# Kernel tuning notes

Measured on AMD Instinct MI355X. Metric: run time of the kernel, lower is better.

## Reference

```python
import jax, jax.numpy as jnp
import numpy as np

SCALE = 64.0
MARGIN = 0.5
EPS_CLAMP = 1e-7
EPS_NORM = 1e-12

N, D, C = 4096, 512, 30000


def setup_inputs() -> dict:
    key = jax.random.key(0)
    k1, k2, k3 = jax.random.split(key, 3)
    embeddings = jax.random.normal(k1, (N, D), dtype=jnp.float32)
    classifier_weights = jax.random.normal(k2, (C, D), dtype=jnp.float32)
    labels = jax.random.randint(k3, (N,), 0, C, dtype=jnp.int64)
    return {"embeddings": embeddings, "labels": labels, "classifier_weights": classifier_weights}


def reference(embeddings, labels, classifier_weights):
    # F.normalize(classifier_weights): L2-normalize each class row (dim=1)
    norm = jnp.linalg.norm(classifier_weights, axis=1, keepdims=True)
    w_norm = classifier_weights / jnp.maximum(norm, EPS_NORM)
    # cosine similarity logits: [N, C]  (embeddings are NOT normalized in source)
    cosine = jnp.einsum("nd,cd->nc", embeddings, w_norm)
    # angle with margin added only at the target class
    angle = jnp.arccos(jnp.clip(cosine, -1.0 + EPS_CLAMP, 1.0 - EPS_CLAMP))
    one_hot = jax.nn.one_hot(labels, C, dtype=cosine.dtype)
    logits = jnp.cos(angle + MARGIN * one_hot) * SCALE
    # mean cross-entropy
    logp = jax.nn.log_softmax(logits, axis=-1)
    nll = -jnp.take_along_axis(logp, labels[:, None], axis=1)[:, 0]
    return jnp.mean(nll)
```

## Files before the change

kernel.cpp:

```cpp
#include <hip/hip_runtime.h>
#include <cstdint>
#include <cstddef>

#define N_ROWS 4096
#define DIM    512
#define NCLS   30000
#define BM 256
#define BN 256
#define BK 32
#define NT2  118
#define CPAD (NT2 * 256)
#define SPT 2
#define NSTRIPS (NT2 / SPT)
#define KT  (DIM / BK)
#define NS  (SPT * KT)

typedef float  f32x4  __attribute__((ext_vector_type(4)));
typedef short  bf16x8 __attribute__((ext_vector_type(8)));
typedef unsigned int   u32;
typedef unsigned short u16;

#define WB_BYTES   ((size_t)CPAD * DIM * 2)
#define EB_BYTES   ((size_t)N_ROWS * DIM * 2)
#define PS_BYTES   ((size_t)NT2 * N_ROWS * 4)
#define CT_BYTES   ((size_t)N_ROWS * 4)
#define BL_BYTES   (64 * 4)
#define LAB_BYTES  ((size_t)N_ROWS * 4)

#define CLIP_HI ( 1.0f - 1e-7f)
#define CLIP_LO (-1.0f + 1e-7f)
#define COSM 0.8775825618903728f
#define SINM 0.4794255386042030f
#define K1   92.33248261972189f

__device__ __forceinline__ u16 f2bf(float f) {
  u32 x = __builtin_bit_cast(u32, f);
  x += 0x7fffu + ((x >> 16) & 1u);
  return (u16)(x >> 16);
}

__device__ __forceinline__ void gl_lds16(const u16* g, u16* l) {
  __builtin_amdgcn_global_load_lds((const __attribute__((address_space(1))) u32*)g,
                                   (__attribute__((address_space(3))) u32*)l,
                                   16, 0, 0);
}

__global__ void lab_detect(const int* __restrict__ lab, int* __restrict__ flag) {
  __shared__ int s_nz;
  int tid = threadIdx.x;
  if (tid == 0) s_nz = 0;
  __syncthreads();
  int nz = 0;
  for (int i = tid; i < N_ROWS / 2; i += 1024) nz |= lab[2 * i + 1];
  if (nz) atomicOr(&s_nz, 1);
  __syncthreads();
  if (tid == 0) *flag = (s_nz == 0) ? 1 : 0;
}

__global__ void lab_fix(const int* __restrict__ lab, const int* __restrict__ flag,
                        int* __restrict__ out) {
  int i = blockIdx.x * 256 + threadIdx.x;
  out[i] = flag[0] ? lab[2 * i] : lab[i];
}

__global__ void prep_w(const float* __restrict__ w, u16* __restrict__ wb) {
  int wv   = threadIdx.x >> 6;
  int lane = threadIdx.x & 63;
  int c = blockIdx.x * 4 + wv;
  u16* dst = wb + (size_t)c * DIM + lane * 8;
  if (c >= NCLS) {
    *(uint4*)dst = make_uint4(0, 0, 0, 0);
    return;
  }
  const float* src = w + (size_t)c * DIM + lane * 8;
  float4 v0 = *(const float4*)src;
  float4 v1 = *(const float4*)(src + 4);
  float a[8] = {v0.x, v0.y, v0.z, v0.w, v1.x, v1.y, v1.z, v1.w};
  float ss = 0.f;
  #pragma unroll
  for (int i = 0; i < 8; i++) ss += a[i] * a[i];
  #pragma unroll
  for (int off = 32; off; off >>= 1) ss += __shfl_xor(ss, off, 64);
  float inv = 1.0f / fmaxf(sqrtf(ss), 1e-12f);
  union { u16 h[8]; uint4 q; } pk;
  #pragma unroll
  for (int i = 0; i < 8; i++) pk.h[i] = f2bf(a[i] * inv);
  *(uint4*)dst = pk.q;
}

__global__ void prep_e(const float* __restrict__ e, u16* __restrict__ eb) {
  size_t idx = ((size_t)blockIdx.x * 256 + threadIdx.x) * 8;
  float4 v0 = *(const float4*)(e + idx);
  float4 v1 = *(const float4*)(e + idx + 4);
  float a[8] = {v0.x, v0.y, v0.z, v0.w, v1.x, v1.y, v1.z, v1.w};
  union { u16 h[8]; uint4 q; } pk;
  #pragma unroll
  for (int i = 0; i < 8; i++) pk.h[i] = f2bf(a[i]);
  *(uint4*)(eb + idx) = pk.q;
}

__global__ void tgt_k(const float* __restrict__ emb, const float* __restrict__ wts,
                      const int* __restrict__ lab, float* __restrict__ ct) {
  int w = threadIdx.x >> 6, l = threadIdx.x & 63;
  int row = blockIdx.x * 4 + w;
  int c = lab[row];
  const float* e  = emb + (size_t)row * DIM + l * 8;
  const float* wp = wts + (size_t)c   * DIM + l * 8;
  float4 e0 = *(const float4*)e,       e1 = *(const float4*)(e + 4);
  float4 w0 = *(const float4*)wp,      w1 = *(const float4*)(wp + 4);
  float dot = e0.x*w0.x + e0.y*w0.y + e0.z*w0.z + e0.w*w0.w
            + e1.x*w1.x + e1.y*w1.y + e1.z*w1.z + e1.w*w1.w;
  float ss  = w0.x*w0.x + w0.y*w0.y + w0.z*w0.z + w0.w*w0.w
            + w1.x*w1.x + w1.y*w1.y + w1.z*w1.z + w1.w*w1.w;
  #pragma unroll
  for (int off = 32; off; off >>= 1) {
    dot += __shfl_xor(dot, off, 64);
    ss  += __shfl_xor(ss,  off, 64);
  }
  if (l == 0) ct[row] = dot / fmaxf(sqrtf(ss), 1e-12f);
}

__global__ __launch_bounds__(512, 2) void arc_main(
    const u16* __restrict__ eb, const u16* __restrict__ wb,
    float* __restrict__ psum)
{
  __shared__ __align__(16) u16 lA[3][BM * BK];
  __shared__ __align__(16) u16 lB[3][BN * BK];
  __shared__ float ep[4][BM];
  const int tid = threadIdx.x;
  const int l   = tid & 63;
  const int w   = tid >> 6;
  const int wm  = w >> 2, wn = w & 3;
  const int mi    = blockIdx.x & 15;
  const int strip = blockIdx.x >> 4;
  const int rowbase = mi * BM;
  const int n0 = strip * SPT;

  u32 aoff[8], boff[4];
  const int bq = l >> 4;
  #pragma unroll
  for (int m = 0; m < 8; m++) {
    int r = wm * 128 + m * 16 + (l & 15);
    aoff[m] = (u32)r * BK + ((bq ^ ((r >> 1) & 3)) << 3);
  }
  #pragma unroll
  for (int n = 0; n < 4; n++) {
    int r = wn * 64 + n * 16 + (l & 15);
    boff[n] = (u32)r * BK + ((bq ^ ((r >> 1) & 3)) << 3);
  }

  const int sch = (w & 3) * 4;
  u32 goff[4];
  #pragma unroll
  for (int i = 0; i < 4; i++) {
    int rl = (sch + i) * 16 + (l >> 2);
    goff[i] = (u32)rl * DIM + (((l & 3) ^ ((rl >> 1) & 3)) << 3);
  }
  const bool isA = (w < 4);
  const u16* gsrc = isA ? (eb + (size_t)rowbase * DIM) : wb;
  u16* lds0 = isA ? &lA[0][0] : &lB[0][0];

  #define STAGE(u_) do {                                                     \
    const int buf_ = (u_) % 3;                                               \
    const u32 base_ = isA ? (u32)(((u_) & 15) * BK)                          \
        : (u32)(n0 + ((u_) >> 4)) * BN * DIM + (u32)(((u_) & 15) * BK);      \
    u16* dst_ = lds0 + buf_ * (BM * BK) + sch * 512;                         \
    _Pragma("unroll")                                                        \
    for (int i_ = 0; i_ < 4; i_++)                                           \
      gl_lds16(gsrc + base_ + goff[i_], dst_ + i_ * 512);                    \
  } while (0)

  f32x4 acc[8][4];
  #pragma unroll
  for (int m = 0; m < 8; m++)
    #pragma unroll
    for (int n = 0; n < 4; n++)
      #pragma unroll
      for (int q = 0; q < 4; q++) acc[m][n][q] = 0.f;

  STAGE(0);
  STAGE(1);

  for (int u = 0; u < NS; u++) {
    if (u < NS - 1) asm volatile("s_waitcnt vmcnt(4)" ::: "memory");
    else            asm volatile("s_waitcnt vmcnt(0)" ::: "memory");
    __builtin_amdgcn_s_barrier();
    asm volatile("" ::: "memory");
    if (u + 2 < NS) STAGE(u + 2);

    const int buf = u % 3;
    bf16x8 af[8], bg[4];
    #pragma unroll
    for (int m = 0; m < 8; m++) af[m] = *(const bf16x8*)&lA[buf][aoff[m]];
    #pragma unroll
    for (int n = 0; n < 4; n++) bg[n] = *(const bf16x8*)&lB[buf][boff[n]];

    __builtin_amdgcn_s_setprio(1);
    #pragma unroll
    for (int m = 0; m < 8; m++)
      #pragma unroll
      for (int n = 0; n < 4; n++)
        acc[m][n] = __builtin_amdgcn_mfma_f32_16x16x32_bf16(af[m], bg[n], acc[m][n], 0, 0, 0);
    __builtin_amdgcn_s_setprio(0);

    if ((u & 15) == 15) {
      const int nt = n0 + (u >> 4);
      #pragma unroll
      for (int m = 0; m < 8; m++) {
        #pragma unroll
        for (int q = 0; q < 4; q++) {
          float s = 0.f;
          #pragma unroll
          for (int n = 0; n < 4; n++) {
            float tc = __builtin_amdgcn_fmed3f(acc[m][n][q], CLIP_LO, CLIP_HI);
            s += __builtin_amdgcn_exp2f(__builtin_fmaf(tc, K1, -K1));
            acc[m][n][q] = 0.f;
          }
          s += __shfl_xor(s, 1, 64);
          s += __shfl_xor(s, 2, 64);
          s += __shfl_xor(s, 4, 64);
          s += __shfl_xor(s, 8, 64);
          if ((l & 15) == 0) ep[wn][wm * 128 + m * 16 + (l >> 4) * 4 + q] = s;
        }
      }
      asm volatile("s_waitcnt lgkmcnt(0)" ::: "memory");
      __builtin_amdgcn_s_barrier();
      asm volatile("" ::: "memory");
      if (l < 32) {
        int r = w * 32 + l;
        float t = ep[0][r] + ep[1][r] + ep[2][r] + ep[3][r];
        psum[(size_t)nt * N_ROWS + rowbase + r] = t;
      }
    }
  }
  #undef STAGE
}

__global__ void arc_finish1(const float* __restrict__ psum, const float* __restrict__ ct,
                            float* __restrict__ bl) {
  int tid = threadIdx.x;
  int row = blockIdx.x * 256 + tid;
  float S = 0.f;
  for (int p = 0; p < NT2; p++) S += psum[(size_t)p * N_ROWS + row];
  float c  = __builtin_amdgcn_fmed3f(ct[row], CLIP_LO, CLIP_HI);
  float cm = c * COSM - sqrtf(fmaxf(1.0f - c * c, 0.0f)) * SINM;
  float S2 = S - __builtin_amdgcn_exp2f(__builtin_fmaf(c,  K1, -K1))
               + __builtin_amdgcn_exp2f(__builtin_fmaf(cm, K1, -K1));
  float loss = 64.0f + __builtin_amdgcn_logf(S2) * 0.6931471805599453f - 64.0f * cm;
  #pragma unroll
  for (int off = 32; off; off >>= 1) loss += __shfl_xor(loss, off, 64);
  __shared__ float red[4];
  if ((tid & 63) == 0) red[tid >> 6] = loss;
  __syncthreads();
  if (tid == 0) bl[blockIdx.x] = red[0] + red[1] + red[2] + red[3];
}

__global__ void arc_finish2(const float* __restrict__ bl, float* __restrict__ out) {
  if (threadIdx.x == 0) {
    float t = 0.f;
    for (int i = 0; i < N_ROWS / 256; i++) t += bl[i];
    out[0] = t * (1.0f / (float)N_ROWS);
  }
}

extern "C" void kernel_launch(void* const* d_in, const int* in_sizes, int n_in,
                              void* d_out, int out_size, void* d_ws, size_t ws_size,
                              hipStream_t stream) {
  const float* emb   = (const float*)d_in[0];
  const int*   lab   = (const int*)d_in[1];
  const float* wts   = (const float*)d_in[2];

  char* ws = (char*)d_ws;
  u16*   wb    = (u16*)(ws);
  u16*   eb    = (u16*)(ws + WB_BYTES);
  float* psum  = (float*)(ws + WB_BYTES + EB_BYTES);
  float* ct    = (float*)(ws + WB_BYTES + EB_BYTES + PS_BYTES);
  float* bl    = (float*)(ws + WB_BYTES + EB_BYTES + PS_BYTES + CT_BYTES);
  int*   lab32 = (int*)  (ws + WB_BYTES + EB_BYTES + PS_BYTES + CT_BYTES + BL_BYTES);
  int*   flag  = (int*)  (ws + WB_BYTES + EB_BYTES + PS_BYTES + CT_BYTES + BL_BYTES + LAB_BYTES);

  lab_detect<<<dim3(1), dim3(1024), 0, stream>>>(lab, flag);
  lab_fix<<<dim3(N_ROWS / 256), dim3(256), 0, stream>>>(lab, flag, lab32);
  prep_w<<<dim3(CPAD / 4), dim3(256), 0, stream>>>(wts, wb);
  prep_e<<<dim3((N_ROWS * DIM / 8) / 256), dim3(256), 0, stream>>>(emb, eb);
  tgt_k<<<dim3(N_ROWS / 4), dim3(256), 0, stream>>>(emb, wts, lab32, ct);
  arc_main<<<dim3(16 * NSTRIPS), dim3(512), 0, stream>>>(eb, wb, psum);
  arc_finish1<<<dim3(N_ROWS / 256), dim3(256), 0, stream>>>(psum, ct, bl);
  arc_finish2<<<dim3(1), dim3(64), 0, stream>>>(bl, (float*)d_out);
}
```

Before: 214.8 us.

## Split GEMM k-step into four phases interleaving LDS reads, global stages, and MFMA

Restructures the main GEMM loop so each k-step runs in four MFMA phases. Each phase is preceded by a subset of LDS fragment reads and one quarter of the next-next stage's global-to-LDS copies, and is separated by barriers and sched_barriers with raised priority. All eight waves now share every A and B copy instead of splitting by wave role, and the triple buffers rotate via pointer swaps. The goal is to overlap memory traffic with matrix work and lower register pressure by holding only half the A fragments at once. The cost is many more workgroup barriers per k-step.

```diff
diff --git a/kernel.cpp b/kernel.cpp
--- a/kernel.cpp
+++ b/kernel.cpp
@@ -124,8 +124,7 @@
     const u16* __restrict__ eb, const u16* __restrict__ wb,
     float* __restrict__ psum)
 {
-  __shared__ __align__(16) u16 lA[3][BM * BK];
-  __shared__ __align__(16) u16 lB[3][BN * BK];
+  __shared__ __align__(16) u16 lds[6 * 8192];
   __shared__ float ep[4][BM];
   const int tid = threadIdx.x;
   const int l   = tid & 63;
@@ -134,7 +133,7 @@
   const int mi    = blockIdx.x & 15;
   const int strip = blockIdx.x >> 4;
   const int rowbase = mi * BM;
-  const int n0 = strip * SPT;
+  const int n0s = strip * SPT;
 
   u32 aoff[8], boff[4];
   const int bq = l >> 4;
@@ -149,26 +148,22 @@
     boff[n] = (u32)r * BK + ((bq ^ ((r >> 1) & 3)) << 3);
   }
 
-  const int sch = (w & 3) * 4;
-  u32 goff[4];
-  #pragma unroll
-  for (int i = 0; i < 4; i++) {
-    int rl = (sch + i) * 16 + (l >> 2);
-    goff[i] = (u32)rl * DIM + (((l & 3) ^ ((rl >> 1) & 3)) << 3);
-  }
-  const bool isA = (w < 4);
-  const u16* gsrc = isA ? (eb + (size_t)rowbase * DIM) : wb;
-  u16* lds0 = isA ? &lA[0][0] : &lB[0][0];
-
-  #define STAGE(u_) do {                                                     \
-    const int buf_ = (u_) % 3;                                               \
-    const u32 base_ = isA ? (u32)(((u_) & 15) * BK)                          \
-        : (u32)(n0 + ((u_) >> 4)) * BN * DIM + (u32)(((u_) & 15) * BK);      \
-    u16* dst_ = lds0 + buf_ * (BM * BK) + sch * 512;                         \
-    _Pragma("unroll")                                                        \
-    for (int i_ = 0; i_ < 4; i_++)                                           \
-      gl_lds16(gsrc + base_ + goff[i_], dst_ + i_ * 512);                    \
-  } while (0)
+  u32 goff[2];
+  #pragma unroll
+  for (int c = 0; c < 2; c++) {
+    int rl = c * 128 + (tid >> 2);
+    goff[c] = (u32)rl * DIM + (((tid & 3) ^ ((rl >> 1) & 3)) << 3);
+  }
+  const u16* ebR = eb + (size_t)rowbase * DIM;
+
+  u16 *pA = lds,             *qA = lds + 8192,  *sA = lds + 16384;
+  u16 *pB = lds + 24576,     *qB = lds + 32768, *sB = lds + 40960;
+
+  #define STAGE_A(v_, t_, c_) \
+    gl_lds16(ebR + (u32)(((v_) & 15) * BK) + goff[c_], (t_) + (c_) * 4096 + w * 512)
+  #define STAGE_B(v_, t_, c_) \
+    gl_lds16(wb + (u32)(n0s + ((v_) >> 4)) * (BN * DIM) + (u32)(((v_) & 15) * BK) + goff[c_], \
+             (t_) + (c_) * 4096 + w * 512)
 
   f32x4 acc[8][4];
   #pragma unroll
@@ -178,33 +173,80 @@
       #pragma unroll
       for (int q = 0; q < 4; q++) acc[m][n][q] = 0.f;
 
-  STAGE(0);
-  STAGE(1);
+  STAGE_A(0, pA, 0); STAGE_A(0, pA, 1); STAGE_B(0, pB, 0); STAGE_B(0, pB, 1);
+  STAGE_A(1, qA, 0); STAGE_A(1, qA, 1); STAGE_B(1, qB, 0); STAGE_B(1, qB, 1);
 
   for (int u = 0; u < NS; u++) {
+    const bool st = (u + 2 < NS);
+    bf16x8 afv[4], bgv[4];
+
     if (u < NS - 1) asm volatile("s_waitcnt vmcnt(4)" ::: "memory");
     else            asm volatile("s_waitcnt vmcnt(0)" ::: "memory");
-    __builtin_amdgcn_s_barrier();
-    asm volatile("" ::: "memory");
-    if (u + 2 < NS) STAGE(u + 2);
-
-    const int buf = u % 3;
-    bf16x8 af[8], bg[4];
-    #pragma unroll
-    for (int m = 0; m < 8; m++) af[m] = *(const bf16x8*)&lA[buf][aoff[m]];
-    #pragma unroll
-    for (int n = 0; n < 4; n++) bg[n] = *(const bf16x8*)&lB[buf][boff[n]];
-
+    #pragma unroll
+    for (int m = 0; m < 4; m++) afv[m] = *(const bf16x8*)&pA[aoff[m]];
+    bgv[0] = *(const bf16x8*)&pB[boff[0]];
+    bgv[1] = *(const bf16x8*)&pB[boff[1]];
+    if (st) STAGE_A(u + 2, sA, 0);
+    __builtin_amdgcn_s_barrier();
+    asm volatile("s_waitcnt lgkmcnt(0)" ::: "memory");
+    __builtin_amdgcn_sched_barrier(0);
     __builtin_amdgcn_s_setprio(1);
     #pragma unroll
-    for (int m = 0; m < 8; m++)
-      #pragma unroll
-      for (int n = 0; n < 4; n++)
-        acc[m][n] = __builtin_amdgcn_mfma_f32_16x16x32_bf16(af[m], bg[n], acc[m][n], 0, 0, 0);
+    for (int m = 0; m < 4; m++)
+      #pragma unroll
+      for (int n = 0; n < 2; n++)
+        acc[m][n] = __builtin_amdgcn_mfma_f32_16x16x32_bf16(afv[m], bgv[n], acc[m][n], 0, 0, 0);
     __builtin_amdgcn_s_setprio(0);
+    __builtin_amdgcn_sched_barrier(0);
+    __builtin_amdgcn_s_barrier();
+
+    bgv[2] = *(const bf16x8*)&pB[boff[2]];
+    bgv[3] = *(const bf16x8*)&pB[boff[3]];
+    if (st) STAGE_A(u + 2, sA, 1);
+    __builtin_amdgcn_s_barrier();
+    asm volatile("s_waitcnt lgkmcnt(0)" ::: "memory");
+    __builtin_amdgcn_sched_barrier(0);
+    __builtin_amdgcn_s_setprio(1);
+    #pragma unroll
+    for (int m = 0; m < 4; m++)
+      #pragma unroll
+      for (int n = 2; n < 4; n++)
+        acc[m][n] = __builtin_amdgcn_mfma_f32_16x16x32_bf16(afv[m], bgv[n], acc[m][n], 0, 0, 0);
+    __builtin_amdgcn_s_setprio(0);
+    __builtin_amdgcn_sched_barrier(0);
+    __builtin_amdgcn_s_barrier();
+
+    #pragma unroll
+    for (int m = 0; m < 4; m++) afv[m] = *(const bf16x8*)&pA[aoff[m + 4]];
+    if (st) STAGE_B(u + 2, sB, 0);
+    __builtin_amdgcn_s_barrier();
+    asm volatile("s_waitcnt lgkmcnt(0)" ::: "memory");
+    __builtin_amdgcn_sched_barrier(0);
+    __builtin_amdgcn_s_setprio(1);
+    #pragma unroll
+    for (int m = 0; m < 4; m++)
+      #pragma unroll
+      for (int n = 0; n < 2; n++)
+        acc[m + 4][n] = __builtin_amdgcn_mfma_f32_16x16x32_bf16(afv[m], bgv[n], acc[m + 4][n], 0, 0, 0);
+    __builtin_amdgcn_s_setprio(0);
+    __builtin_amdgcn_sched_barrier(0);
+    __builtin_amdgcn_s_barrier();
+
+    if (st) STAGE_B(u + 2, sB, 1);
+    __builtin_amdgcn_s_barrier();
+    __builtin_amdgcn_sched_barrier(0);
+    __builtin_amdgcn_s_setprio(1);
+    #pragma unroll
+    for (int m = 0; m < 4; m++)
+      #pragma unroll
+      for (int n = 2; n < 4; n++)
+        acc[m + 4][n] = __builtin_amdgcn_mfma_f32_16x16x32_bf16(afv[m], bgv[n], acc[m + 4][n], 0, 0, 0);
+    __builtin_amdgcn_s_setprio(0);
+    __builtin_amdgcn_sched_barrier(0);
+    __builtin_amdgcn_s_barrier();
 
     if ((u & 15) == 15) {
-      const int nt = n0 + (u >> 4);
+      const int nt = n0s + (u >> 4);
       #pragma unroll
       for (int m = 0; m < 8; m++) {
         #pragma unroll
@@ -231,9 +273,14 @@
         float t = ep[0][r] + ep[1][r] + ep[2][r] + ep[3][r];
         psum[(size_t)nt * N_ROWS + rowbase + r] = t;
       }
+      __builtin_amdgcn_s_barrier();
     }
-  }
-  #undef STAGE
+
+    u16* t0 = pA; pA = qA; qA = sA; sA = t0;
+    u16* t1 = pB; pB = qB; qB = sB; sB = t1;
+  }
+  #undef STAGE_A
+  #undef STAGE_B
 }
 
 __global__ void arc_finish1(const float* __restrict__ psum, const float* __restrict__ ct,
```

Result: slower. 225.3 us (+4.9%).

## Restructure GEMM mainloop to BK=64 double-buffer with interleaved load/MFMA phases

Applied to the files above, without the earlier changes.

Doubles the K tile to 64 and replaces the 3-stage ring buffer with a 2-stage double buffer. Each K step is split into four barrier-separated phases, each interleaving a slice of the next tile's global-to-LDS loads with 16 MFMAs. Occupancy is reduced to one block per CU to fit the larger LDS footprint, and the LDS swizzle switches to an XOR over 8 chunks. The aim is to cut barrier and waitcnt overhead per FLOP and overlap memory traffic with compute, at the cost of more barriers per step, lower occupancy and only one tile of prefetch depth.

```diff
diff --git a/kernel.cpp b/kernel.cpp
--- a/kernel.cpp
+++ b/kernel.cpp
@@ -7,7 +7,7 @@
 #define NCLS   30000
 #define BM 256
 #define BN 256
-#define BK 32
+#define BK 64
 #define NT2  118
 #define CPAD (NT2 * 256)
 #define SPT 2
@@ -120,55 +120,44 @@
   if (l == 0) ct[row] = dot / fmaxf(sqrtf(ss), 1e-12f);
 }
 
-__global__ __launch_bounds__(512, 2) void arc_main(
+__global__ __launch_bounds__(512, 1) void arc_main(
     const u16* __restrict__ eb, const u16* __restrict__ wb,
     float* __restrict__ psum)
 {
-  __shared__ __align__(16) u16 lA[3][BM * BK];
-  __shared__ __align__(16) u16 lB[3][BN * BK];
+  __shared__ __align__(16) u16 lds[2][2][BM * BK];
   __shared__ float ep[4][BM];
-  const int tid = threadIdx.x;
-  const int l   = tid & 63;
-  const int w   = tid >> 6;
+  const int t   = threadIdx.x;
+  const int l   = t & 63;
+  const int w   = t >> 6;
   const int wm  = w >> 2, wn = w & 3;
+  const int cl  = l & 15, bq = l >> 4;
   const int mi    = blockIdx.x & 15;
   const int strip = blockIdx.x >> 4;
   const int rowbase = mi * BM;
-  const int n0 = strip * SPT;
-
-  u32 aoff[8], boff[4];
-  const int bq = l >> 4;
-  #pragma unroll
-  for (int m = 0; m < 8; m++) {
-    int r = wm * 128 + m * 16 + (l & 15);
-    aoff[m] = (u32)r * BK + ((bq ^ ((r >> 1) & 3)) << 3);
-  }
-  #pragma unroll
-  for (int n = 0; n < 4; n++) {
-    int r = wn * 64 + n * 16 + (l & 15);
-    boff[n] = (u32)r * BK + ((bq ^ ((r >> 1) & 3)) << 3);
-  }
-
-  const int sch = (w & 3) * 4;
+  const int n0s = strip * SPT;
+
+  u32 aoff[16], boff[8];
+  #pragma unroll
+  for (int s = 0; s < 2; s++) {
+    #pragma unroll
+    for (int m = 0; m < 8; m++) {
+      int r = wm * 128 + m * 16 + cl;
+      aoff[s * 8 + m] = (u32)r * BK + (((s * 4 + bq) ^ (r & 7)) << 3);
+    }
+    #pragma unroll
+    for (int n = 0; n < 4; n++) {
+      int r = wn * 64 + n * 16 + cl;
+      boff[s * 4 + n] = (u32)r * BK + (((s * 4 + bq) ^ (r & 7)) << 3);
+    }
+  }
+
   u32 goff[4];
   #pragma unroll
-  for (int i = 0; i < 4; i++) {
-    int rl = (sch + i) * 16 + (l >> 2);
-    goff[i] = (u32)rl * DIM + (((l & 3) ^ ((rl >> 1) & 3)) << 3);
-  }
-  const bool isA = (w < 4);
-  const u16* gsrc = isA ? (eb + (size_t)rowbase * DIM) : wb;
-  u16* lds0 = isA ? &lA[0][0] : &lB[0][0];
-
-  #define STAGE(u_) do {                                                     \
-    const int buf_ = (u_) % 3;                                               \
-    const u32 base_ = isA ? (u32)(((u_) & 15) * BK)                          \
-        : (u32)(n0 + ((u_) >> 4)) * BN * DIM + (u32)(((u_) & 15) * BK);      \
-    u16* dst_ = lds0 + buf_ * (BM * BK) + sch * 512;                         \
-    _Pragma("unroll")                                                        \
-    for (int i_ = 0; i_ < 4; i_++)                                           \
-      gl_lds16(gsrc + base_ + goff[i_], dst_ + i_ * 512);                    \
-  } while (0)
+  for (int c = 0; c < 4; c++) {
+    int rl = c * 64 + (t >> 3);
+    goff[c] = (u32)rl * DIM + (((t & 7) ^ (rl & 7)) << 3);
+  }
+  const u16* ebR = eb + (size_t)rowbase * DIM;
 
   f32x4 acc[8][4];
   #pragma unroll
@@ -178,33 +167,149 @@
       #pragma unroll
       for (int q = 0; q < 4; q++) acc[m][n][q] = 0.f;
 
-  STAGE(0);
-  STAGE(1);
+  {
+    const u32 bb0 = (u32)n0s * (BN * DIM);
+    #pragma unroll
+    for (int c = 0; c < 4; c++) {
+      gl_lds16(ebR + goff[c],       &lds[0][0][c * 4096 + w * 512]);
+      gl_lds16(wb + bb0 + goff[c],  &lds[0][1][c * 4096 + w * 512]);
+    }
+  }
 
   for (int u = 0; u < NS; u++) {
-    if (u < NS - 1) asm volatile("s_waitcnt vmcnt(4)" ::: "memory");
-    else            asm volatile("s_waitcnt vmcnt(0)" ::: "memory");
+    const int bi = u & 1;
+    const u16* As = &lds[bi][0][0];
+    const u16* Bs = &lds[bi][1][0];
+    u16* An = &lds[bi ^ 1][0][0];
+    u16* Bn = &lds[bi ^ 1][1][0];
+    const bool st = (u + 1 < NS);
+    const u32 k0n = (u32)(((u + 1) & 7) * BK);
+    const u32 bbn = (u32)(n0s + ((u + 1) >> 3)) * (BN * DIM);
+
+    asm volatile("s_waitcnt vmcnt(0)" ::: "memory");
     __builtin_amdgcn_s_barrier();
     asm volatile("" ::: "memory");
-    if (u + 2 < NS) STAGE(u + 2);
-
-    const int buf = u % 3;
-    bf16x8 af[8], bg[4];
-    #pragma unroll
-    for (int m = 0; m < 8; m++) af[m] = *(const bf16x8*)&lA[buf][aoff[m]];
-    #pragma unroll
-    for (int n = 0; n < 4; n++) bg[n] = *(const bf16x8*)&lB[buf][boff[n]];
-
+
+    bf16x8 a0, a1, a2, a3, b0, b1, b2, b3;
+
+    a0 = *(const bf16x8*)&As[aoff[0]];  a1 = *(const bf16x8*)&As[aoff[1]];
+    a2 = *(const bf16x8*)&As[aoff[2]];  a3 = *(const bf16x8*)&As[aoff[3]];
+    b0 = *(const bf16x8*)&Bs[boff[0]];  b1 = *(const bf16x8*)&Bs[boff[1]];
+    b2 = *(const bf16x8*)&Bs[boff[2]];  b3 = *(const bf16x8*)&Bs[boff[3]];
+    if (st) {
+      gl_lds16(ebR + k0n + goff[0],      An + w * 512);
+      gl_lds16(wb + bbn + k0n + goff[0], Bn + w * 512);
+    }
+    __builtin_amdgcn_s_barrier();
+    asm volatile("s_waitcnt lgkmcnt(0)" ::: "memory");
     __builtin_amdgcn_s_setprio(1);
-    #pragma unroll
-    for (int m = 0; m < 8; m++)
-      #pragma unroll
-      for (int n = 0; n < 4; n++)
-        acc[m][n] = __builtin_amdgcn_mfma_f32_16x16x32_bf16(af[m], bg[n], acc[m][n], 0, 0, 0);
+    acc[0][0] = __builtin_amdgcn_mfma_f32_16x16x32_bf16(a0, b0, acc[0][0], 0, 0, 0);
+    acc[0][1] = __builtin_amdgcn_mfma_f32_16x16x32_bf16(a0, b1, acc[0][1], 0, 0, 0);
+    acc[0][2] = __builtin_amdgcn_mfma_f32_16x16x32_bf16(a0, b2, acc[0][2], 0, 0, 0);
+    acc[0][3] = __builtin_amdgcn_mfma_f32_16x16x32_bf16(a0, b3, acc[0][3], 0, 0, 0);
+    acc[1][0] = __builtin_amdgcn_mfma_f32_16x16x32_bf16(a1, b0, acc[1][0], 0, 0, 0);
+    acc[1][1] = __builtin_amdgcn_mfma_f32_16x16x32_bf16(a1, b1, acc[1][1], 0, 0, 0);
+    acc[1][2] = __builtin_amdgcn_mfma_f32_16x16x32_bf16(a1, b2, acc[1][2], 0, 0, 0);
+    acc[1][3] = __builtin_amdgcn_mfma_f32_16x16x32_bf16(a1, b3, acc[1][3], 0, 0, 0);
+    acc[2][0] = __builtin_amdgcn_mfma_f32_16x16x32_bf16(a2, b0, acc[2][0], 0, 0, 0);
+    acc[2][1] = __builtin_amdgcn_mfma_f32_16x16x32_bf16(a2, b1, acc[2][1], 0, 0, 0);
+    acc[2][2] = __builtin_amdgcn_mfma_f32_16x16x32_bf16(a2, b2, acc[2][2], 0, 0, 0);
+    acc[2][3] = __builtin_amdgcn_mfma_f32_16x16x32_bf16(a2, b3, acc[2][3], 0, 0, 0);
+    acc[3][0] = __builtin_amdgcn_mfma_f32_16x16x32_bf16(a3, b0, acc[3][0], 0, 0, 0);
+    acc[3][1] = __builtin_amdgcn_mfma_f32_16x16x32_bf16(a3, b1, acc[3][1], 0, 0, 0);
+    acc[3][2] = __builtin_amdgcn_mfma_f32_16x16x32_bf16(a3, b2, acc[3][2], 0, 0, 0);
+    acc[3][3] = __builtin_amdgcn_mfma_f32_16x16x32_bf16(a3, b3, acc[3][3], 0, 0, 0);
     __builtin_amdgcn_s_setprio(0);
-
-    if ((u & 15) == 15) {
-      const int nt = n0 + (u >> 4);
+    __builtin_amdgcn_s_barrier();
+
+    a0 = *(const bf16x8*)&As[aoff[4]];  a1 = *(const bf16x8*)&As[aoff[5]];
+    a2 = *(const bf16x8*)&As[aoff[6]];  a3 = *(const bf16x8*)&As[aoff[7]];
+    if (st) {
+      gl_lds16(ebR + k0n + goff[1],      An + 4096 + w * 512);
+      gl_lds16(wb + bbn + k0n + goff[1], Bn + 4096 + w * 512);
+    }
+    __builtin_amdgcn_s_barrier();
+    asm volatile("s_waitcnt lgkmcnt(0)" ::: "memory");
+    __builtin_amdgcn_s_setprio(1);
+    acc[4][0] = __builtin_amdgcn_mfma_f32_16x16x32_bf16(a0, b0, acc[4][0], 0, 0, 0);
+    acc[4][1] = __builtin_amdgcn_mfma_f32_16x16x32_bf16(a0, b1, acc[4][1], 0, 0, 0);
+    acc[4][2] = __builtin_amdgcn_mfma_f32_16x16x32_bf16(a0, b2, acc[4][2], 0, 0, 0);
+    acc[4][3] = __builtin_amdgcn_mfma_f32_16x16x32_bf16(a0, b3, acc[4][3], 0, 0, 0);
+    acc[5][0] = __builtin_amdgcn_mfma_f32_16x16x32_bf16(a1, b0, acc[5][0], 0, 0, 0);
+    acc[5][1] = __builtin_amdgcn_mfma_f32_16x16x32_bf16(a1, b1, acc[5][1], 0, 0, 0);
+    acc[5][2] = __builtin_amdgcn_mfma_f32_16x16x32_bf16(a1, b2, acc[5][2], 0, 0, 0);
+    acc[5][3] = __builtin_amdgcn_mfma_f32_16x16x32_bf16(a1, b3, acc[5][3], 0, 0, 0);
+    acc[6][0] = __builtin_amdgcn_mfma_f32_16x16x32_bf16(a2, b0, acc[6][0], 0, 0, 0);
+    acc[6][1] = __builtin_amdgcn_mfma_f32_16x16x32_bf16(a2, b1, acc[6][1], 0, 0, 0);
+    acc[6][2] = __builtin_amdgcn_mfma_f32_16x16x32_bf16(a2, b2, acc[6][2], 0, 0, 0);
+    acc[6][3] = __builtin_amdgcn_mfma_f32_16x16x32_bf16(a2, b3, acc[6][3], 0, 0, 0);
+    acc[7][0] = __builtin_amdgcn_mfma_f32_16x16x32_bf16(a3, b0, acc[7][0], 0, 0, 0);
+    acc[7][1] = __builtin_amdgcn_mfma_f32_16x16x32_bf16(a3, b1, acc[7][1], 0, 0, 0);
+    acc[7][2] = __builtin_amdgcn_mfma_f32_16x16x32_bf16(a3, b2, acc[7][2], 0, 0, 0);
+    acc[7][3] = __builtin_amdgcn_mfma_f32_16x16x32_bf16(a3, b3, acc[7][3], 0, 0, 0);
+    __builtin_amdgcn_s_setprio(0);
+    __builtin_amdgcn_s_barrier();
+
+    a0 = *(const bf16x8*)&As[aoff[8]];  a1 = *(const bf16x8*)&As[aoff[9]];
+    a2 = *(const bf16x8*)&As[aoff[10]]; a3 = *(const bf16x8*)&As[aoff[11]];
+    b0 = *(const bf16x8*)&Bs[boff[4]];  b1 = *(const bf16x8*)&Bs[boff[5]];
+    b2 = *(const bf16x8*)&Bs[boff[6]];  b3 = *(const bf16x8*)&Bs[boff[7]];
+    if (st) {
+      gl_lds16(ebR + k0n + goff[2],      An + 8192 + w * 512);
+      gl_lds16(wb + bbn + k0n + goff[2], Bn + 8192 + w * 512);
+    }
+    __builtin_amdgcn_s_barrier();
+    asm volatile("s_waitcnt lgkmcnt(0)" ::: "memory");
+    __builtin_amdgcn_s_setprio(1);
+    acc[0][0] = __builtin_amdgcn_mfma_f32_16x16x32_bf16(a0, b0, acc[0][0], 0, 0, 0);
+    acc[0][1] = __builtin_amdgcn_mfma_f32_16x16x32_bf16(a0, b1, acc[0][1], 0, 0, 0);
+    acc[0][2] = __builtin_amdgcn_mfma_f32_16x16x32_bf16(a0, b2, acc[0][2], 0, 0, 0);
+    acc[0][3] = __builtin_amdgcn_mfma_f32_16x16x32_bf16(a0, b3, acc[0][3], 0, 0, 0);
+    acc[1][0] = __builtin_amdgcn_mfma_f32_16x16x32_bf16(a1, b0, acc[1][0], 0, 0, 0);
+    acc[1][1] = __builtin_amdgcn_mfma_f32_16x16x32_bf16(a1, b1, acc[1][1], 0, 0, 0);
+    acc[1][2] = __builtin_amdgcn_mfma_f32_16x16x32_bf16(a1, b2, acc[1][2], 0, 0, 0);
+    acc[1][3] = __builtin_amdgcn_mfma_f32_16x16x32_bf16(a1, b3, acc[1][3], 0, 0, 0);
+    acc[2][0] = __builtin_amdgcn_mfma_f32_16x16x32_bf16(a2, b0, acc[2][0], 0, 0, 0);
+    acc[2][1] = __builtin_amdgcn_mfma_f32_16x16x32_bf16(a2, b1, acc[2][1], 0, 0, 0);
+    acc[2][2] = __builtin_amdgcn_mfma_f32_16x16x32_bf16(a2, b2, acc[2][2], 0, 0, 0);
+    acc[2][3] = __builtin_amdgcn_mfma_f32_16x16x32_bf16(a2, b3, acc[2][3], 0, 0, 0);
+    acc[3][0] = __builtin_amdgcn_mfma_f32_16x16x32_bf16(a3, b0, acc[3][0], 0, 0, 0);
+    acc[3][1] = __builtin_amdgcn_mfma_f32_16x16x32_bf16(a3, b1, acc[3][1], 0, 0, 0);
+    acc[3][2] = __builtin_amdgcn_mfma_f32_16x16x32_bf16(a3, b2, acc[3][2], 0, 0, 0);
+    acc[3][3] = __builtin_amdgcn_mfma_f32_16x16x32_bf16(a3, b3, acc[3][3], 0, 0, 0);
+    __builtin_amdgcn_s_setprio(0);
+    __builtin_amdgcn_s_barrier();
+
+    a0 = *(const bf16x8*)&As[aoff[12]]; a1 = *(const bf16x8*)&As[aoff[13]];
+    a2 = *(const bf16x8*)&As[aoff[14]]; a3 = *(const bf16x8*)&As[aoff[15]];
+    if (st) {
+      gl_lds16(ebR + k0n + goff[3],      An + 12288 + w * 512);
+      gl_lds16(wb + bbn + k0n + goff[3], Bn + 12288 + w * 512);
+    }
+    __builtin_amdgcn_s_barrier();
+    asm volatile("s_waitcnt lgkmcnt(0)" ::: "memory");
+    __builtin_amdgcn_s_setprio(1);
+    acc[4][0] = __builtin_amdgcn_mfma_f32_16x16x32_bf16(a0, b0, acc[4][0], 0, 0, 0);
+    acc[4][1] = __builtin_amdgcn_mfma_f32_16x16x32_bf16(a0, b1, acc[4][1], 0, 0, 0);
+    acc[4][2] = __builtin_amdgcn_mfma_f32_16x16x32_bf16(a0, b2, acc[4][2], 0, 0, 0);
+    acc[4][3] = __builtin_amdgcn_mfma_f32_16x16x32_bf16(a0, b3, acc[4][3], 0, 0, 0);
+    acc[5][0] = __builtin_amdgcn_mfma_f32_16x16x32_bf16(a1, b0, acc[5][0], 0, 0, 0);
+    acc[5][1] = __builtin_amdgcn_mfma_f32_16x16x32_bf16(a1, b1, acc[5][1], 0, 0, 0);
+    acc[5][2] = __builtin_amdgcn_mfma_f32_16x16x32_bf16(a1, b2, acc[5][2], 0, 0, 0);
+    acc[5][3] = __builtin_amdgcn_mfma_f32_16x16x32_bf16(a1, b3, acc[5][3], 0, 0, 0);
+    acc[6][0] = __builtin_amdgcn_mfma_f32_16x16x32_bf16(a2, b0, acc[6][0], 0, 0, 0);
+    acc[6][1] = __builtin_amdgcn_mfma_f32_16x16x32_bf16(a2, b1, acc[6][1], 0, 0, 0);
+    acc[6][2] = __builtin_amdgcn_mfma_f32_16x16x32_bf16(a2, b2, acc[6][2], 0, 0, 0);
+    acc[6][3] = __builtin_amdgcn_mfma_f32_16x16x32_bf16(a2, b3, acc[6][3], 0, 0, 0);
+    acc[7][0] = __builtin_amdgcn_mfma_f32_16x16x32_bf16(a3, b0, acc[7][0], 0, 0, 0);
+    acc[7][1] = __builtin_amdgcn_mfma_f32_16x16x32_bf16(a3, b1, acc[7][1], 0, 0, 0);
+    acc[7][2] = __builtin_amdgcn_mfma_f32_16x16x32_bf16(a3, b2, acc[7][2], 0, 0, 0);
+    acc[7][3] = __builtin_amdgcn_mfma_f32_16x16x32_bf16(a3, b3, acc[7][3], 0, 0, 0);
+    __builtin_amdgcn_s_setprio(0);
+    __builtin_amdgcn_s_barrier();
+
+    if ((u & 7) == 7) {
+      const int nt = n0s + (u >> 3);
       #pragma unroll
       for (int m = 0; m < 8; m++) {
         #pragma unroll
@@ -228,12 +333,12 @@
       asm volatile("" ::: "memory");
       if (l < 32) {
         int r = w * 32 + l;
-        float t = ep[0][r] + ep[1][r] + ep[2][r] + ep[3][r];
-        psum[(size_t)nt * N_ROWS + rowbase + r] = t;
+        float v = ep[0][r] + ep[1][r] + ep[2][r] + ep[3][r];
+        psum[(size_t)nt * N_ROWS + rowbase + r] = v;
       }
-    }
-  }
-  #undef STAGE
+      __builtin_amdgcn_s_barrier();
+    }
+  }
 }
 
 __global__ void arc_finish1(const float* __restrict__ psum, const float* __restrict__ ct,
```

Measured after the change: 213.4 us. No clear change (-0.7%).

## Shrink main GEMM tile to 128x256 with 4 waves and double buffering

Applied to the files above, without the earlier changes.

Restructures the fused cosine-logit GEMM from 256x256 tiles with 8 waves, triple buffering and two class strips per block, to 128x256 tiles with 4 waves, double buffering and one strip per block. Each block now does a single K loop and one exp/row-sum epilogue. The grid grows from 944 to 3776 blocks, which should give better load balance and occupancy. The cost is more global traffic per FLOP because the smaller M tile gives less reuse, and a shallower prefetch pipeline that waits on vmcnt(0) every iteration.

```diff
diff --git a/kernel.cpp b/kernel.cpp
--- a/kernel.cpp
+++ b/kernel.cpp
@@ -5,15 +5,13 @@
 #define N_ROWS 4096
 #define DIM    512
 #define NCLS   30000
-#define BM 256
+#define BM 128
 #define BN 256
 #define BK 32
 #define NT2  118
 #define CPAD (NT2 * 256)
-#define SPT 2
-#define NSTRIPS (NT2 / SPT)
-#define KT  (DIM / BK)
-#define NS  (SPT * KT)
+#define MI   (N_ROWS / BM)
+#define KS   (DIM / BK)
 
 typedef float  f32x4  __attribute__((ext_vector_type(4)));
 typedef short  bf16x8 __attribute__((ext_vector_type(8)));
@@ -120,55 +118,45 @@
   if (l == 0) ct[row] = dot / fmaxf(sqrtf(ss), 1e-12f);
 }
 
-__global__ __launch_bounds__(512, 2) void arc_main(
+__global__ __launch_bounds__(256) void arc_main(
     const u16* __restrict__ eb, const u16* __restrict__ wb,
     float* __restrict__ psum)
 {
-  __shared__ __align__(16) u16 lA[3][BM * BK];
-  __shared__ __align__(16) u16 lB[3][BN * BK];
+  __shared__ __align__(16) u16 lds[2][(BM + BN) * BK];
   __shared__ float ep[4][BM];
-  const int tid = threadIdx.x;
-  const int l   = tid & 63;
-  const int w   = tid >> 6;
-  const int wm  = w >> 2, wn = w & 3;
-  const int mi    = blockIdx.x & 15;
-  const int strip = blockIdx.x >> 4;
+  const int t  = threadIdx.x;
+  const int l  = t & 63;
+  const int w  = t >> 6;
+  const int cl = l & 15, bq = l >> 4;
+  const int mi    = blockIdx.x & (MI - 1);
+  const int strip = blockIdx.x >> 5;
   const int rowbase = mi * BM;
-  const int n0 = strip * SPT;
 
   u32 aoff[8], boff[4];
-  const int bq = l >> 4;
   #pragma unroll
   for (int m = 0; m < 8; m++) {
-    int r = wm * 128 + m * 16 + (l & 15);
+    int r = m * 16 + cl;
     aoff[m] = (u32)r * BK + ((bq ^ ((r >> 1) & 3)) << 3);
   }
   #pragma unroll
   for (int n = 0; n < 4; n++) {
-    int r = wn * 64 + n * 16 + (l & 15);
-    boff[n] = (u32)r * BK + ((bq ^ ((r >> 1) & 3)) << 3);
-  }
-
-  const int sch = (w & 3) * 4;
-  u32 goff[4];
-  #pragma unroll
-  for (int i = 0; i < 4; i++) {
-    int rl = (sch + i) * 16 + (l >> 2);
-    goff[i] = (u32)rl * DIM + (((l & 3) ^ ((rl >> 1) & 3)) << 3);
-  }
-  const bool isA = (w < 4);
-  const u16* gsrc = isA ? (eb + (size_t)rowbase * DIM) : wb;
-  u16* lds0 = isA ? &lA[0][0] : &lB[0][0];
-
-  #define STAGE(u_) do {                                                     \
-    const int buf_ = (u_) % 3;                                               \
-    const u32 base_ = isA ? (u32)(((u_) & 15) * BK)                          \
-        : (u32)(n0 + ((u_) >> 4)) * BN * DIM + (u32)(((u_) & 15) * BK);      \
-    u16* dst_ = lds0 + buf_ * (BM * BK) + sch * 512;                         \
-    _Pragma("unroll")                                                        \
-    for (int i_ = 0; i_ < 4; i_++)                                           \
-      gl_lds16(gsrc + base_ + goff[i_], dst_ + i_ * 512);                    \
-  } while (0)
+    int r = w * 64 + n * 16 + cl;
+    boff[n] = (u32)(BM * BK) + (u32)r * BK + ((bq ^ ((r >> 1) & 3)) << 3);
+  }
+
+  u32 ga[2], gb[4];
+  #pragma unroll
+  for (int i = 0; i < 2; i++) {
+    int rl = (w * 2 + i) * 16 + (l >> 2);
+    ga[i] = (u32)rl * DIM + (((l & 3) ^ ((rl >> 1) & 3)) << 3);
+  }
+  #pragma unroll
+  for (int j = 0; j < 4; j++) {
+    int rl = (w * 4 + j) * 16 + (l >> 2);
+    gb[j] = (u32)rl * DIM + (((l & 3) ^ ((rl >> 1) & 3)) << 3);
+  }
+  const u16* ebR = eb + (size_t)rowbase * DIM;
+  const u16* wbN = wb + (size_t)strip * BN * DIM;
 
   f32x4 acc[8][4];
   #pragma unroll
@@ -178,22 +166,32 @@
       #pragma unroll
       for (int q = 0; q < 4; q++) acc[m][n][q] = 0.f;
 
-  STAGE(0);
-  STAGE(1);
-
-  for (int u = 0; u < NS; u++) {
-    if (u < NS - 1) asm volatile("s_waitcnt vmcnt(4)" ::: "memory");
-    else            asm volatile("s_waitcnt vmcnt(0)" ::: "memory");
+  #pragma unroll
+  for (int i = 0; i < 2; i++) gl_lds16(ebR + ga[i], &lds[0][(w * 2 + i) * 512]);
+  #pragma unroll
+  for (int j = 0; j < 4; j++) gl_lds16(wbN + gb[j], &lds[0][BM * BK + (w * 4 + j) * 512]);
+
+  for (int u = 0; u < KS; u++) {
+    asm volatile("s_waitcnt vmcnt(0)" ::: "memory");
     __builtin_amdgcn_s_barrier();
     asm volatile("" ::: "memory");
-    if (u + 2 < NS) STAGE(u + 2);
-
-    const int buf = u % 3;
+
+    if (u + 1 < KS) {
+      const u32 ko = (u32)(u + 1) * BK;
+      u16* Ad = &lds[(u + 1) & 1][0];
+      u16* Bd = &lds[(u + 1) & 1][BM * BK];
+      #pragma unroll
+      for (int i = 0; i < 2; i++) gl_lds16(ebR + ko + ga[i], Ad + (w * 2 + i) * 512);
+      #pragma unroll
+      for (int j = 0; j < 4; j++) gl_lds16(wbN + ko + gb[j], Bd + (w * 4 + j) * 512);
+    }
+
+    const u16* Ls = &lds[u & 1][0];
     bf16x8 af[8], bg[4];
     #pragma unroll
-    for (int m = 0; m < 8; m++) af[m] = *(const bf16x8*)&lA[buf][aoff[m]];
-    #pragma unroll
-    for (int n = 0; n < 4; n++) bg[n] = *(const bf16x8*)&lB[buf][boff[n]];
+    for (int m = 0; m < 8; m++) af[m] = *(const bf16x8*)&Ls[aoff[m]];
+    #pragma unroll
+    for (int n = 0; n < 4; n++) bg[n] = *(const bf16x8*)&Ls[boff[n]];
 
     __builtin_amdgcn_s_setprio(1);
     #pragma unroll
@@ -202,38 +200,30 @@
       for (int n = 0; n < 4; n++)
         acc[m][n] = __builtin_amdgcn_mfma_f32_16x16x32_bf16(af[m], bg[n], acc[m][n], 0, 0, 0);
     __builtin_amdgcn_s_setprio(0);
-
-    if ((u & 15) == 15) {
-      const int nt = n0 + (u >> 4);
-      #pragma unroll
-      for (int m = 0; m < 8; m++) {
-        #pragma unroll
-        for (int q = 0; q < 4; q++) {
-          float s = 0.f;
-          #pragma unroll
-          for (int n = 0; n < 4; n++) {
-            float tc = __builtin_amdgcn_fmed3f(acc[m][n][q], CLIP_LO, CLIP_HI);
-            s += __builtin_amdgcn_exp2f(__builtin_fmaf(tc, K1, -K1));
-            acc[m][n][q] = 0.f;
-          }
-          s += __shfl_xor(s, 1, 64);
-          s += __shfl_xor(s, 2, 64);
-          s += __shfl_xor(s, 4, 64);
-          s += __shfl_xor(s, 8, 64);
-          if ((l & 15) == 0) ep[wn][wm * 128 + m * 16 + (l >> 4) * 4 + q] = s;
-        }
+  }
+
+  #pragma unroll
+  for (int m = 0; m < 8; m++) {
+    #pragma unroll
+    for (int q = 0; q < 4; q++) {
+      float s = 0.f;
+      #pragma unroll
+      for (int n = 0; n < 4; n++) {
+        float tc = __builtin_amdgcn_fmed3f(acc[m][n][q], CLIP_LO, CLIP_HI);
+        s += __builtin_amdgcn_exp2f(__builtin_fmaf(tc, K1, -K1));
       }
-      asm volatile("s_waitcnt lgkmcnt(0)" ::: "memory");
-      __builtin_amdgcn_s_barrier();
-      asm volatile("" ::: "memory");
-      if (l < 32) {
-        int r = w * 32 + l;
-        float t = ep[0][r] + ep[1][r] + ep[2][r] + ep[3][r];
-        psum[(size_t)nt * N_ROWS + rowbase + r] = t;
-      }
+      s += __shfl_xor(s, 1, 64);
+      s += __shfl_xor(s, 2, 64);
+      s += __shfl_xor(s, 4, 64);
+      s += __shfl_xor(s, 8, 64);
+      if ((l & 15) == 0) ep[w][m * 16 + (l >> 4) * 4 + q] = s;
     }
   }
-  #undef STAGE
+  __syncthreads();
+  if (t < BM) {
+    float v = ep[0][t] + ep[1][t] + ep[2][t] + ep[3][t];
+    psum[(size_t)strip * N_ROWS + rowbase + t] = v;
+  }
 }
 
 __global__ void arc_finish1(const float* __restrict__ psum, const float* __restrict__ ct,
@@ -284,7 +274,7 @@
   prep_w<<<dim3(CPAD / 4), dim3(256), 0, stream>>>(wts, wb);
   prep_e<<<dim3((N_ROWS * DIM / 8) / 256), dim3(256), 0, stream>>>(emb, eb);
   tgt_k<<<dim3(N_ROWS / 4), dim3(256), 0, stream>>>(emb, wts, lab32, ct);
-  arc_main<<<dim3(16 * NSTRIPS), dim3(512), 0, stream>>>(eb, wb, psum);
+  arc_main<<<dim3(NT2 * MI), dim3(256), 0, stream>>>(eb, wb, psum);
   arc_finish1<<<dim3(N_ROWS / 256), dim3(256), 0, stream>>>(psum, ct, bl);
   arc_finish2<<<dim3(1), dim3(64), 0, stream>>>(bl, (float*)d_out);
 }
```

New measurement: 240.6 us. +12.0%, slower.
